# Performance work log

Measured on AMD Instinct MI355X. Metric: run time of the kernel, lower is better.

The kernel has to match this reference:

```python
import jax, jax.numpy as jnp
import numpy as np
import math

BLOCK = 256
NUM_HEADS = 32
HEAD_DIM = 128
HIDDEN = 2048
INNER = NUM_HEADS * HEAD_DIM
SEQ = 4096
EPS = 1e-5
LAYER_IDX = 0
NUM_LAYERS = 32


def _build_slopes(n):
    def get_slopes(n):
        def pow2(m):
            start = 2 ** (-2 ** (-(math.log2(m) - 3)))
            return [start * start ** i for i in range(m)]
        if math.log2(n).is_integer():
            return pow2(n)
        c = 2 ** math.floor(math.log2(n))
        return pow2(c) + get_slopes(2 * c)[0::2][: n - c]
    s = np.asarray(get_slopes(n), dtype=np.float32).reshape(n, 1, 1)
    # layer decay scaling as in __init__
    s = s * (1.0 - LAYER_IDX / (NUM_LAYERS - 1) + 1e-5)
    return s


def setup_inputs() -> dict:
    key = jax.random.key(0)
    k1, k2, k3, k4 = jax.random.split(key, 4)
    sd_h = 1.0 / math.sqrt(HIDDEN)
    sd_i = 1.0 / math.sqrt(INNER)
    return {
        "hidden_states": jax.random.normal(k1, (SEQ, HIDDEN), jnp.float32),
        "w_qkv": jax.random.normal(k2, (HIDDEN, 3 * INNER), jnp.float32) * sd_h,
        "w_gate": jax.random.normal(k3, (HIDDEN, INNER), jnp.float32) * sd_h,
        "w_out": jax.random.normal(k4, (INNER, HIDDEN), jnp.float32) * sd_i,
        "norm_weight": jnp.ones((INNER,), jnp.float32),
        "slope_rate": jnp.asarray(_build_slopes(NUM_HEADS)),
        "kv_cache": jnp.zeros((NUM_HEADS, HEAD_DIM, HEAD_DIM), jnp.float32),
    }


def _lightning_attention(q, k, v, slope, kv0):
    # q,k,v: [h, n, d]; slope: [h,1,1]; kv0: [h, d, d]
    h, n, d = q.shape
    nb = n // BLOCK
    qb = q.reshape(h, nb, BLOCK, d).transpose(1, 0, 2, 3)  # [nb,h,B,d]
    kb = k.reshape(h, nb, BLOCK, d).transpose(1, 0, 2, 3)
    vb = v.reshape(h, nb, BLOCK, d).transpose(1, 0, 2, 3)

    idx = jnp.arange(BLOCK, dtype=jnp.float32)
    diff = idx[:, None] - idx[None, :]                      # i - j
    s = slope.reshape(h, 1, 1)
    intra_decay = jnp.where(diff >= 0, jnp.exp(-s * diff), 0.0)   # [h,B,B]
    q_decay = jnp.exp(-s * (idx + 1.0).reshape(1, BLOCK, 1))      # [h,B,1]
    k_decay = jnp.exp(-s * (BLOCK - 1.0 - idx).reshape(1, BLOCK, 1))  # [h,B,1]
    block_decay = jnp.exp(-s * BLOCK)                             # [h,1,1]

    def step(kv, blk):
        qc, kc, vc = blk  # each [h,B,d]
        scores = jnp.einsum('hid,hjd->hij', qc, kc) * intra_decay
        o_intra = jnp.einsum('hij,hjd->hid', scores, vc)
        o_inter = q_decay * jnp.einsum('hid,hde->hie', qc, kv)
        kv_new = block_decay * kv + jnp.einsum('hjd,hje->hde', kc * k_decay, vc)
        return kv_new, o_intra + o_inter

    kv_final, outs = jax.lax.scan(step, kv0, (qb, kb, vb))
    out = outs.transpose(1, 0, 2, 3).reshape(h, n, d)
    return out, kv_final


def reference(hidden_states, w_qkv, w_gate, w_out, norm_weight, slope_rate, kv_cache):
    n = hidden_states.shape[0]
    # qkv projection + SiLU activation (done in fp32 in the original)
    qkv = jax.nn.silu(hidden_states @ w_qkv)                  # [n, 3*inner]
    qkv = qkv.reshape(n, NUM_HEADS, 3 * HEAD_DIM)
    q, k, v = jnp.split(qkv, 3, axis=-1)                      # [n,h,d] each
    q = q.transpose(1, 0, 2)                                  # [h,n,d]
    k = k.transpose(1, 0, 2)
    v = v.transpose(1, 0, 2)

    attn, kv_final = _lightning_attention(q, k, v, slope_rate, kv_cache)
    attn = attn.transpose(1, 0, 2).reshape(n, INNER)          # n (h d)

    # RMSNorm (fp32) then sigmoid gate then output projection
    var = jnp.mean(attn * attn, axis=-1, keepdims=True)
    normed = attn * jax.lax.rsqrt(var + EPS) * norm_weight
    gate = jax.nn.sigmoid(hidden_states @ w_gate)
    out = (gate * normed) @ w_out                             # [n, hidden]
    return out
```

## Files before the change

kernel.cpp:

```cpp
#include <hip/hip_runtime.h>
#include <stdint.h>

typedef __bf16 bf16x8 __attribute__((ext_vector_type(8)));
typedef float  f32x4  __attribute__((ext_vector_type(4)));
typedef unsigned short u16x8 __attribute__((ext_vector_type(8)));

__device__ __forceinline__ unsigned short f2bf(float f) {
    union { float f; uint32_t u; } x; x.f = f;
    uint32_t r = (x.u + 0x7FFFu + ((x.u >> 16) & 1u)) >> 16;
    return (unsigned short)r;
}
__device__ __forceinline__ float bf2f(unsigned short b) {
    union { uint32_t u; float f; } x; x.u = ((uint32_t)b) << 16;
    return x.f;
}

__device__ __forceinline__ void gl16(const void* g, void* l) {
    __builtin_amdgcn_global_load_lds(
        (const __attribute__((address_space(1))) void*)g,
        (__attribute__((address_space(3))) void*)(uint32_t)(uintptr_t)l,
        16, 0, 0);
}

#define MFMA16(a, b, c) __builtin_amdgcn_mfma_f32_16x16x32_bf16((a), (b), (c), 0, 0, 0)

__global__ __launch_bounds__(256) void f32_to_bf16_kernel(const float* __restrict__ in,
                                                          unsigned short* __restrict__ out,
                                                          int n8) {
    int i = blockIdx.x * 256 + threadIdx.x;
    if (i >= n8) return;
    float4 a = ((const float4*)in)[2 * i];
    float4 b = ((const float4*)in)[2 * i + 1];
    u16x8 o;
    o[0] = f2bf(a.x); o[1] = f2bf(a.y); o[2] = f2bf(a.z); o[3] = f2bf(a.w);
    o[4] = f2bf(b.x); o[5] = f2bf(b.y); o[6] = f2bf(b.z); o[7] = f2bf(b.w);
    ((u16x8*)out)[i] = o;
}

__global__ __launch_bounds__(256) void transpose_w_kernel(const float* __restrict__ in,
                                                          unsigned short* __restrict__ out,
                                                          int R, int C) {
    __shared__ float tile[32][33];
    int c0 = blockIdx.x * 32, r0 = blockIdx.y * 32;
    int lx = threadIdx.x & 31, ly = threadIdx.x >> 5;
#pragma unroll
    for (int i = ly; i < 32; i += 8)
        tile[i][lx] = in[(size_t)(r0 + i) * C + c0 + lx];
    __syncthreads();
#pragma unroll
    for (int i = ly; i < 32; i += 8)
        out[(size_t)(c0 + i) * R + r0 + lx] = f2bf(tile[lx][i]);
}

template <int ACT, int OUTF32>
__global__ __launch_bounds__(512, 2) void gemm256_kernel(const unsigned short* __restrict__ A,
                                                         const unsigned short* __restrict__ Bt,
                                                         void* __restrict__ Cout,
                                                         int N, int K, int NBN) {
    __shared__ unsigned short Abuf[2][2][8192];
    __shared__ unsigned short Bbuf[2][2][8192];

    int nwg = gridDim.x;
    int bid = blockIdx.x;
    int wg = (bid & 7) * (nwg >> 3) + (bid >> 3);
    int bm = wg / NBN, bn = wg % NBN;
    int tid = threadIdx.x, lane = tid & 63, w = tid >> 6;
    int wr = w >> 2, wc = w & 3;

    int r0 = tid >> 3;
    int cbs = (tid & 7) << 4;
    int el0 = (cbs ^ ((r0 & 7) << 4)) >> 1;
    int r1 = 64 + r0;
    int el1 = (cbs ^ ((r1 & 7) << 4)) >> 1;
    int lo0 = tid * 16, lo1 = 8192 + tid * 16;

    const unsigned short* Ag0 = A + (size_t)(bm * 256) * K;
    const unsigned short* Ag1 = A + (size_t)(bm * 256 + 128) * K;
    const unsigned short* Bg0 = Bt + (size_t)(bn * 256) * K;
    const unsigned short* Bg1 = Bt + (size_t)(bn * 256 + 128) * K;

#define STAGE(src, dstHalf, k0)                                            \
    do {                                                                   \
        gl16((src) + (size_t)r0 * K + (k0) + el0, (char*)(dstHalf) + lo0); \
        gl16((src) + (size_t)r1 * K + (k0) + el1, (char*)(dstHalf) + lo1); \
    } while (0)

    int aRow = wr * 64 + (lane & 15);
    int bRow = wc * 32 + (lane & 15);
    int swz = (lane & 7) << 4;
    int cbb = (lane >> 4) << 4;

#define RD_A(slot, R, m, kk) \
    af[R][m][kk] = *(const bf16x8*)((const char*)Abuf[slot][R] + ((aRow + (m) * 16) << 7) + (((kk) * 64 + cbb) ^ swz))
#define RD_B(slot, Cq, n, kk) \
    bfr[Cq][n][kk] = *(const bf16x8*)((const char*)Bbuf[slot][Cq] + ((bRow + (n) * 16) << 7) + (((kk) * 64 + cbb) ^ swz))

#define QUAD(q, Rh, Cc)                                                       \
    do {                                                                      \
        _Pragma("unroll")                                                     \
        for (int m = 0; m < 4; ++m)                                           \
            _Pragma("unroll")                                                 \
            for (int n = 0; n < 2; ++n) {                                     \
                acc[q][m][n] = MFMA16(af[Rh][m][0], bfr[Cc][n][0], acc[q][m][n]); \
                acc[q][m][n] = MFMA16(af[Rh][m][1], bfr[Cc][n][1], acc[q][m][n]); \
            }                                                                 \
    } while (0)

    bf16x8 af[2][4][2];
    bf16x8 bfr[2][2][2];
    f32x4 acc[4][4][2];
#pragma unroll
    for (int q = 0; q < 4; ++q)
#pragma unroll
        for (int m = 0; m < 4; ++m)
#pragma unroll
            for (int n = 0; n < 2; ++n)
#pragma unroll
                for (int r = 0; r < 4; ++r) acc[q][m][n][r] = 0.f;

    int NT = K >> 6;
    STAGE(Ag0, Abuf[0][0], 0);
    STAGE(Bg0, Bbuf[0][0], 0);
    STAGE(Ag1, Abuf[0][1], 0);
    STAGE(Bg1, Bbuf[0][1], 0);
    STAGE(Ag0, Abuf[1][0], 64);
    STAGE(Bg0, Bbuf[1][0], 64);
    STAGE(Ag1, Abuf[1][1], 64);
    STAGE(Bg1, Bbuf[1][1], 64);
    asm volatile("s_waitcnt vmcnt(8)" ::: "memory");
    __builtin_amdgcn_s_barrier();
#pragma unroll
    for (int m = 0; m < 4; ++m) { RD_A(0, 0, m, 0); RD_A(0, 0, m, 1); }
#pragma unroll
    for (int n = 0; n < 2; ++n) { RD_B(0, 0, n, 0); RD_B(0, 0, n, 1); }

    for (int t = 0; t < NT; ++t) {
        int cur = t & 1, nx = cur ^ 1;
        bool rd = (t + 1 < NT);
        bool st = (t + 2 < NT);
        int ks = (t + 2) << 6;

#pragma unroll
        for (int m = 0; m < 4; ++m) { RD_A(cur, 1, m, 0); RD_A(cur, 1, m, 1); }
        asm volatile("s_waitcnt lgkmcnt(8)" ::: "memory");
        __builtin_amdgcn_sched_barrier(0);
        __builtin_amdgcn_s_setprio(1);
        QUAD(0, 0, 0);
        __builtin_amdgcn_s_setprio(0);

#pragma unroll
        for (int n = 0; n < 2; ++n) { RD_B(cur, 1, n, 0); RD_B(cur, 1, n, 1); }
        asm volatile("s_waitcnt lgkmcnt(4)" ::: "memory");
        __builtin_amdgcn_sched_barrier(0);
        __builtin_amdgcn_s_setprio(1);
        QUAD(1, 1, 0);
        __builtin_amdgcn_s_setprio(0);

        asm volatile("s_waitcnt lgkmcnt(0)" ::: "memory");
        asm volatile("s_waitcnt vmcnt(0)" ::: "memory");
        __builtin_amdgcn_s_barrier();
        if (st) {
            STAGE(Ag0, Abuf[cur][0], ks);
            STAGE(Bg0, Bbuf[cur][0], ks);
        }
        if (rd) {
#pragma unroll
            for (int n = 0; n < 2; ++n) { RD_B(nx, 0, n, 0); RD_B(nx, 0, n, 1); }
        }
        __builtin_amdgcn_s_setprio(1);
        QUAD(2, 0, 1);
        __builtin_amdgcn_s_setprio(0);

        if (st) {
            STAGE(Ag1, Abuf[cur][1], ks);
            STAGE(Bg1, Bbuf[cur][1], ks);
        }
        if (rd) {
#pragma unroll
            for (int m = 0; m < 4; ++m) { RD_A(nx, 0, m, 0); RD_A(nx, 0, m, 1); }
        }
        __builtin_amdgcn_s_setprio(1);
        QUAD(3, 1, 1);
        __builtin_amdgcn_s_setprio(0);
    }

#pragma unroll
    for (int q = 0; q < 4; ++q) {
        const int R_ = q & 1, C_ = q >> 1;
#pragma unroll
        for (int m = 0; m < 4; ++m) {
            int row0 = bm * 256 + R_ * 128 + wr * 64 + m * 16 + ((lane >> 4) * 4);
#pragma unroll
            for (int n = 0; n < 2; ++n) {
                int col = bn * 256 + C_ * 128 + wc * 32 + n * 16 + (lane & 15);
#pragma unroll
                for (int rg = 0; rg < 4; ++rg) {
                    float v = acc[q][m][n][rg];
                    if (ACT == 1) v = v / (1.f + __expf(-v));
                    else if (ACT == 2) v = 1.f / (1.f + __expf(-v));
                    size_t idx = (size_t)(row0 + rg) * N + col;
                    if (OUTF32) ((float*)Cout)[idx] = v;
                    else        ((unsigned short*)Cout)[idx] = f2bf(v);
                }
            }
        }
    }
#undef STAGE
#undef RD_A
#undef RD_B
#undef QUAD
}

__global__ __launch_bounds__(256) void kv_transpose_kernel(const unsigned short* __restrict__ qkv,
                                                           const float* __restrict__ slopes,
                                                           unsigned short* __restrict__ kts,
                                                           unsigned short* __restrict__ vt) {
    __shared__ unsigned short tk[32][33];
    __shared__ unsigned short tv[32][33];
    int n0 = blockIdx.x * 32, d0 = blockIdx.y * 32, h = blockIdx.z;
    float s = slopes[h];
    int lx = threadIdx.x & 31, ly = threadIdx.x >> 5;
#pragma unroll
    for (int i = ly; i < 32; i += 8) {
        int n = n0 + i;
        size_t rowb = (size_t)n * 12288 + h * 384;
        float kv = bf2f(qkv[rowb + 128 + d0 + lx]) * __expf(-s * (float)(255 - (n & 255)));
        tk[i][lx] = f2bf(kv);
        tv[i][lx] = qkv[rowb + 256 + d0 + lx];
    }
    __syncthreads();
#pragma unroll
    for (int i = ly; i < 32; i += 8) {
        size_t ob = (size_t)(h * 128 + d0 + i) * 4096 + n0 + lx;
        kts[ob] = tk[lx][i];
        vt[ob] = tv[lx][i];
    }
}

__global__ __launch_bounds__(256) void kv_outer_kernel(const unsigned short* __restrict__ kts,
                                                       const unsigned short* __restrict__ vt,
                                                       float* __restrict__ U) {
    __shared__ unsigned short Kc[128 * 64];
    __shared__ unsigned short Vc[128 * 64];
    int blk = blockIdx.x;
    int h = blk & 31, t = blk >> 5;
    int tid = threadIdx.x, lane = tid & 63, w = tid >> 6;

    f32x4 acc[2][8];
#pragma unroll
    for (int m = 0; m < 2; ++m)
#pragma unroll
        for (int n = 0; n < 8; ++n)
#pragma unroll
            for (int r = 0; r < 4; ++r) acc[m][n][r] = 0.f;

    for (int ks = 0; ks < 4; ++ks) {
        __syncthreads();
#pragma unroll
        for (int it = 0; it < 4; ++it) {
            int slot = it * 256 + tid;
            int o = slot * 16;
            int r = o >> 7;
            int cb = o & 127;
            int scb = cb ^ ((r & 7) << 4);
            size_t j = (size_t)t * 256 + ks * 64 + (scb >> 1);
            gl16(kts + (size_t)(h * 128 + r) * 4096 + j, (char*)Kc + o);
            gl16(vt + (size_t)(h * 128 + r) * 4096 + j, (char*)Vc + o);
        }
        __syncthreads();
#pragma unroll
        for (int kk = 0; kk < 2; ++kk) {
            int kb = kk * 64 + ((lane >> 4) * 16);
            bf16x8 vf[2], kf[8];
#pragma unroll
            for (int m = 0; m < 2; ++m) {
                int e = w * 32 + m * 16 + (lane & 15);
                vf[m] = *(const bf16x8*)((const char*)Vc + (e << 7) + (kb ^ ((e & 7) << 4)));
            }
#pragma unroll
            for (int n = 0; n < 8; ++n) {
                int d = n * 16 + (lane & 15);
                kf[n] = *(const bf16x8*)((const char*)Kc + (d << 7) + (kb ^ ((d & 7) << 4)));
            }
#pragma unroll
            for (int m = 0; m < 2; ++m)
#pragma unroll
                for (int n = 0; n < 8; ++n)
                    acc[m][n] = MFMA16(vf[m], kf[n], acc[m][n]);
        }
    }
    size_t base = (size_t)(h * 16 + t) * 16384;
#pragma unroll
    for (int m = 0; m < 2; ++m)
#pragma unroll
        for (int n = 0; n < 8; ++n)
#pragma unroll
            for (int r = 0; r < 4; ++r) {
                int e = w * 32 + m * 16 + ((lane >> 4) * 4) + r;
                int d = n * 16 + (lane & 15);
                U[base + (size_t)e * 128 + d] = acc[m][n][r];
            }
}

__global__ __launch_bounds__(256) void kv_scan_kernel(const float* __restrict__ kv_cache,
                                                      const float* __restrict__ U,
                                                      const float* __restrict__ slopes,
                                                      unsigned short* __restrict__ Wb) {
    int h = blockIdx.x >> 3;
    int c0 = (blockIdx.x & 7) * 2048;
    int tid = threadIdx.x;
    float s = slopes[h];
    float bd = __expf(-s * 256.f);
    float wst[8];
    size_t hb = (size_t)h * 16384;
#pragma unroll
    for (int i = 0; i < 8; ++i) {
        int idx = c0 + i * 256 + tid;
        int e = idx >> 7, d = idx & 127;
        wst[i] = kv_cache[hb + (size_t)d * 128 + e];
    }
    for (int t = 0; t < 16; ++t) {
        size_t base = (size_t)(h * 16 + t) * 16384 + c0;
#pragma unroll
        for (int i = 0; i < 8; ++i) {
            int idx = i * 256 + tid;
            Wb[base + idx] = f2bf(wst[i]);
            wst[i] = bd * wst[i] + U[base + idx];
        }
    }
}

__global__ __launch_bounds__(256, 1) void attn_out_kernel(const unsigned short* __restrict__ qkv,
                                                          const unsigned short* __restrict__ vt,
                                                          const unsigned short* __restrict__ Wb,
                                                          const float* __restrict__ slopes,
                                                          unsigned short* __restrict__ attn) {
    __shared__ unsigned short lds[65536];
    unsigned short* Qs = lds;
    unsigned short* Ps = lds + 32768;
    unsigned short* KW = lds + 49152;
    unsigned short* Ks = KW;
    unsigned short* Vs = KW + 8192;

    int blk = blockIdx.x;
    int h = blk & 31, t = blk >> 5;
    float s = slopes[h];
    int tid = threadIdx.x, lane = tid & 63, w = tid >> 6;

#pragma unroll
    for (int it = 0; it < 16; ++it) {
        int slot = it * 256 + tid;
        int o = slot * 16;
        int r = o >> 8, cb = o & 255, scb = cb ^ ((r & 7) << 4);
        gl16(qkv + (size_t)(t * 256 + r) * 12288 + h * 384 + (scb >> 1), (char*)Qs + o);
    }
#pragma unroll
    for (int it = 0; it < 8; ++it) {
        int slot = it * 256 + tid;
        int o = slot * 16;
        int e = o >> 8, cb = o & 255, scb = cb ^ ((e & 7) << 4);
        gl16(Wb + (size_t)((h * 16 + t) * 128 + e) * 128 + (scb >> 1), (char*)KW + o);
    }
    __syncthreads();

    f32x4 acc[4][8];
#pragma unroll
    for (int m = 0; m < 4; ++m)
#pragma unroll
        for (int n = 0; n < 8; ++n)
#pragma unroll
            for (int r = 0; r < 4; ++r) acc[m][n][r] = 0.f;

#pragma unroll
    for (int kk = 0; kk < 4; ++kk) {
        int kb = kk * 64 + ((lane >> 4) * 16);
        bf16x8 qf[4], wf[8];
#pragma unroll
        for (int m = 0; m < 4; ++m) {
            int r = w * 64 + m * 16 + (lane & 15);
            qf[m] = *(const bf16x8*)((const char*)Qs + (r << 8) + (kb ^ ((r & 7) << 4)));
        }
#pragma unroll
        for (int n = 0; n < 8; ++n) {
            int e = n * 16 + (lane & 15);
            wf[n] = *(const bf16x8*)((const char*)KW + (e << 8) + (kb ^ ((e & 7) << 4)));
        }
#pragma unroll
        for (int m = 0; m < 4; ++m)
#pragma unroll
            for (int n = 0; n < 8; ++n)
                acc[m][n] = MFMA16(qf[m], wf[n], acc[m][n]);
    }
#pragma unroll
    for (int m = 0; m < 4; ++m)
#pragma unroll
        for (int rg = 0; rg < 4; ++rg) {
            int i = w * 64 + m * 16 + ((lane >> 4) * 4) + rg;
            float qd = __expf(-s * (float)(i + 1));
#pragma unroll
            for (int n = 0; n < 8; ++n) acc[m][n][rg] *= qd;
        }

    for (int jb = 0; jb < 4; ++jb) {
        __syncthreads();
#pragma unroll
        for (int it = 0; it < 4; ++it) {
            int slot = it * 256 + tid;
            int o = slot * 16;
            int r = o >> 8, cb = o & 255, scb = cb ^ ((r & 7) << 4);
            gl16(qkv + (size_t)(t * 256 + jb * 64 + r) * 12288 + h * 384 + 128 + (scb >> 1),
                 (char*)Ks + o);
        }
#pragma unroll
        for (int it = 0; it < 4; ++it) {
            int slot = it * 256 + tid;
            int o = slot * 16;
            int e = o >> 7, cb = o & 127, scb = cb ^ ((e & 7) << 4);
            gl16(vt + (size_t)(h * 128 + e) * 4096 + t * 256 + jb * 64 + (scb >> 1),
                 (char*)Vs + o);
        }
        __syncthreads();

        if (jb <= w) {
            f32x4 sc[4][4];
#pragma unroll
            for (int m = 0; m < 4; ++m)
#pragma unroll
                for (int n = 0; n < 4; ++n)
#pragma unroll
                    for (int r = 0; r < 4; ++r) sc[m][n][r] = 0.f;
#pragma unroll
            for (int kk = 0; kk < 4; ++kk) {
                int kb = kk * 64 + ((lane >> 4) * 16);
                bf16x8 qf[4], kf[4];
#pragma unroll
                for (int m = 0; m < 4; ++m) {
                    int r = w * 64 + m * 16 + (lane & 15);
                    qf[m] = *(const bf16x8*)((const char*)Qs + (r << 8) + (kb ^ ((r & 7) << 4)));
                }
#pragma unroll
                for (int n = 0; n < 4; ++n) {
                    int r = n * 16 + (lane & 15);
                    kf[n] = *(const bf16x8*)((const char*)Ks + (r << 8) + (kb ^ ((r & 7) << 4)));
                }
#pragma unroll
                for (int m = 0; m < 4; ++m)
#pragma unroll
                    for (int n = 0; n < 4; ++n)
                        sc[m][n] = MFMA16(qf[m], kf[n], sc[m][n]);
            }
            unsigned short* Pw = Ps + w * 4096;
#pragma unroll
            for (int m = 0; m < 4; ++m)
#pragma unroll
                for (int n = 0; n < 4; ++n)
#pragma unroll
                    for (int rg = 0; rg < 4; ++rg) {
                        int il = m * 16 + ((lane >> 4) * 4) + rg;
                        int i = w * 64 + il;
                        int jl = n * 16 + (lane & 15);
                        int j = jb * 64 + jl;
                        float v = 0.f;
                        if (i >= j) v = sc[m][n][rg] * __expf(-s * (float)(i - j));
                        int cb2 = (jl * 2) ^ ((il & 7) << 4);
                        *(unsigned short*)((char*)Pw + (il << 7) + cb2) = f2bf(v);
                    }
            asm volatile("s_waitcnt lgkmcnt(0)" ::: "memory");
#pragma unroll
            for (int kk = 0; kk < 2; ++kk) {
                int kb = kk * 64 + ((lane >> 4) * 16);
                bf16x8 pf[4], vf[8];
#pragma unroll
                for (int m = 0; m < 4; ++m) {
                    int il = m * 16 + (lane & 15);
                    pf[m] = *(const bf16x8*)((const char*)Pw + (il << 7) + (kb ^ ((il & 7) << 4)));
                }
#pragma unroll
                for (int n = 0; n < 8; ++n) {
                    int e = n * 16 + (lane & 15);
                    vf[n] = *(const bf16x8*)((const char*)Vs + (e << 7) + (kb ^ ((e & 7) << 4)));
                }
#pragma unroll
                for (int m = 0; m < 4; ++m)
#pragma unroll
                    for (int n = 0; n < 8; ++n)
                        acc[m][n] = MFMA16(pf[m], vf[n], acc[m][n]);
            }
        }
    }

#pragma unroll
    for (int m = 0; m < 4; ++m)
#pragma unroll
        for (int n = 0; n < 8; ++n)
#pragma unroll
            for (int rg = 0; rg < 4; ++rg) {
                int i = w * 64 + m * 16 + ((lane >> 4) * 4) + rg;
                int col = h * 128 + n * 16 + (lane & 15);
                attn[(size_t)(t * 256 + i) * 4096 + col] = f2bf(acc[m][n][rg]);
            }
}

__global__ __launch_bounds__(256) void rms_gate_kernel(const unsigned short* __restrict__ attn,
                                                       const unsigned short* __restrict__ gate,
                                                       const float* __restrict__ nw,
                                                       unsigned short* __restrict__ gated) {
    int row = blockIdx.x, tid = threadIdx.x;
    int lane = tid & 63, w = tid >> 6;
    const unsigned short* ar = attn + (size_t)row * 4096 + tid * 16;
    u16x8 a0 = *(const u16x8*)ar;
    u16x8 a1 = *(const u16x8*)(ar + 8);
    float v[16];
    float ss = 0.f;
#pragma unroll
    for (int j = 0; j < 8; ++j) { v[j] = bf2f(a0[j]); v[8 + j] = bf2f(a1[j]); }
#pragma unroll
    for (int j = 0; j < 16; ++j) ss += v[j] * v[j];
#pragma unroll
    for (int o = 32; o > 0; o >>= 1) ss += __shfl_xor(ss, o);
    __shared__ float red[4];
    if (lane == 0) red[w] = ss;
    __syncthreads();
    float tot = red[0] + red[1] + red[2] + red[3];
    float rs = rsqrtf(tot * (1.f / 4096.f) + 1e-5f);
    const unsigned short* gr = gate + (size_t)row * 4096 + tid * 16;
    u16x8 g0 = *(const u16x8*)gr;
    u16x8 g1 = *(const u16x8*)(gr + 8);
    const float* nwp = nw + tid * 16;
    u16x8 o0, o1;
#pragma unroll
    for (int j = 0; j < 8; ++j) {
        o0[j] = f2bf(v[j] * rs * nwp[j] * bf2f(g0[j]));
        o1[j] = f2bf(v[8 + j] * rs * nwp[8 + j] * bf2f(g1[j]));
    }
    unsigned short* gp = gated + (size_t)row * 4096 + tid * 16;
    *(u16x8*)gp = o0;
    *(u16x8*)(gp + 8) = o1;
}

extern "C" void kernel_launch(void* const* d_in, const int* in_sizes, int n_in,
                              void* d_out, int out_size, void* d_ws, size_t ws_size,
                              hipStream_t stream) {
    const float* hs       = (const float*)d_in[0];
    const float* w_qkv    = (const float*)d_in[1];
    const float* w_gate   = (const float*)d_in[2];
    const float* w_out    = (const float*)d_in[3];
    const float* nw       = (const float*)d_in[4];
    const float* slopes   = (const float*)d_in[5];
    const float* kv_cache = (const float*)d_in[6];
    float* out = (float*)d_out;
    char* ws = (char*)d_ws;

    unsigned short* hsb  = (unsigned short*)(ws + 0);
    unsigned short* wqt  = (unsigned short*)(ws + 16777216);
    unsigned short* wgt  = (unsigned short*)(ws + 67108864);
    unsigned short* wot  = (unsigned short*)(ws + 83886080);
    unsigned short* qkv  = (unsigned short*)(ws + 100663296);
    unsigned short* gate = (unsigned short*)(ws + 201326592);
    unsigned short* kts  = (unsigned short*)(ws + 234881024);
    unsigned short* vt   = (unsigned short*)(ws + 268435456);
    float*          U    = (float*)(ws + 301989888);
    unsigned short* Wb   = (unsigned short*)(ws + 335544320);
    unsigned short* attn  = wqt;
    unsigned short* gated = qkv;

    f32_to_bf16_kernel<<<4096, 256, 0, stream>>>(hs, hsb, 1048576);
    {
        dim3 g(384, 64);
        transpose_w_kernel<<<g, 256, 0, stream>>>(w_qkv, wqt, 2048, 12288);
    }
    {
        dim3 g(128, 64);
        transpose_w_kernel<<<g, 256, 0, stream>>>(w_gate, wgt, 2048, 4096);
    }
    {
        dim3 g(64, 128);
        transpose_w_kernel<<<g, 256, 0, stream>>>(w_out, wot, 4096, 2048);
    }
    gemm256_kernel<1, 0><<<768, 512, 0, stream>>>(hsb, wqt, qkv, 12288, 2048, 48);
    gemm256_kernel<2, 0><<<256, 512, 0, stream>>>(hsb, wgt, gate, 4096, 2048, 16);
    {
        dim3 g(128, 4, 32);
        kv_transpose_kernel<<<g, 256, 0, stream>>>(qkv, slopes, kts, vt);
    }
    kv_outer_kernel<<<512, 256, 0, stream>>>(kts, vt, U);
    kv_scan_kernel<<<256, 256, 0, stream>>>(kv_cache, U, slopes, Wb);
    attn_out_kernel<<<512, 256, 0, stream>>>(qkv, vt, Wb, slopes, attn);
    rms_gate_kernel<<<4096, 256, 0, stream>>>(attn, gate, nw, gated);
    gemm256_kernel<0, 1><<<128, 512, 0, stream>>>(gated, wot, out, 2048, 4096, 8);
}
```

Before: 567.1 us.

## Remap GEMM tiles, split attention query tiles, add small-tile output GEMM

The large GEMM's block-to-tile mapping is changed so that each XCD covers a compact group of M and N tiles, which should improve L2 reuse. The output projection moves from a 128-block 256x256 GEMM to a new 128x128-tile GEMM with 512 blocks, so more CUs are busy; the new kernel has no double buffering. attn_out now splits each 256-row query block into two 128-row halves, doubling the grid and halving LDS so two blocks fit per CU. kv_scan stages the transposed kv_cache read through LDS so the global loads are coalesced.

```diff
diff --git a/kernel.cpp b/kernel.cpp
--- a/kernel.cpp
+++ b/kernel.cpp
@@ -60,10 +60,10 @@
     __shared__ unsigned short Abuf[2][2][8192];
     __shared__ unsigned short Bbuf[2][2][8192];
 
-    int nwg = gridDim.x;
     int bid = blockIdx.x;
-    int wg = (bid & 7) * (nwg >> 3) + (bid >> 3);
-    int bm = wg / NBN, bn = wg % NBN;
+    int xcd = bid & 7, kw = bid >> 3;
+    int bm = (xcd & 3) * 4 + (kw & 3);
+    int bn = (xcd >> 2) * (NBN >> 1) + (kw >> 2);
     int tid = threadIdx.x, lane = tid & 63, w = tid >> 6;
     int wr = w >> 2, wc = w & 3;
 
@@ -211,6 +211,82 @@
 #undef QUAD
 }
 
+template <int ACT, int OUTBF>
+__global__ __launch_bounds__(256) void gemm_bt_kernel(const unsigned short* __restrict__ A,
+                                                      const unsigned short* __restrict__ Bt,
+                                                      void* __restrict__ Cp,
+                                                      int M, int N, int K) {
+    __shared__ unsigned short As[128 * 64];
+    __shared__ unsigned short Bs[128 * 64];
+    int bn = blockIdx.x, bm = blockIdx.y;
+    int tid = threadIdx.x, lane = tid & 63, w = tid >> 6;
+    int wr = w >> 1, wc = w & 1;
+
+    f32x4 acc[4][4];
+#pragma unroll
+    for (int m = 0; m < 4; ++m)
+#pragma unroll
+        for (int n = 0; n < 4; ++n)
+#pragma unroll
+            for (int r = 0; r < 4; ++r) acc[m][n][r] = 0.f;
+
+    const size_t Abase = (size_t)bm * 128 * K;
+    const size_t Bbase = (size_t)bn * 128 * K;
+
+    for (int k0 = 0; k0 < K; k0 += 64) {
+        __syncthreads();
+#pragma unroll
+        for (int it = 0; it < 4; ++it) {
+            int slot = it * 256 + tid;
+            int o = slot * 16;
+            int r = o >> 7;
+            int cb = o & 127;
+            int scb = cb ^ ((r & 7) << 4);
+            gl16(A + Abase + (size_t)r * K + k0 + (scb >> 1), (char*)As + o);
+            gl16(Bt + Bbase + (size_t)r * K + k0 + (scb >> 1), (char*)Bs + o);
+        }
+        __syncthreads();
+#pragma unroll
+        for (int kk = 0; kk < 2; ++kk) {
+            int kb = kk * 64 + ((lane >> 4) * 16);
+            bf16x8 af[4], bfr[4];
+#pragma unroll
+            for (int m = 0; m < 4; ++m) {
+                int r = wr * 64 + m * 16 + (lane & 15);
+                af[m] = *(const bf16x8*)((const char*)As + (r << 7) + (kb ^ ((r & 7) << 4)));
+            }
+#pragma unroll
+            for (int n = 0; n < 4; ++n) {
+                int r = wc * 64 + n * 16 + (lane & 15);
+                bfr[n] = *(const bf16x8*)((const char*)Bs + (r << 7) + (kb ^ ((r & 7) << 4)));
+            }
+#pragma unroll
+            for (int m = 0; m < 4; ++m)
+#pragma unroll
+                for (int n = 0; n < 4; ++n)
+                    acc[m][n] = MFMA16(af[m], bfr[n], acc[m][n]);
+        }
+    }
+
+#pragma unroll
+    for (int m = 0; m < 4; ++m) {
+        int rowb = bm * 128 + wr * 64 + m * 16 + ((lane >> 4) * 4);
+#pragma unroll
+        for (int n = 0; n < 4; ++n) {
+            int col = bn * 128 + wc * 64 + n * 16 + (lane & 15);
+#pragma unroll
+            for (int r = 0; r < 4; ++r) {
+                float v = acc[m][n][r];
+                if (ACT == 1) v = v / (1.f + __expf(-v));
+                else if (ACT == 2) v = 1.f / (1.f + __expf(-v));
+                size_t idx = (size_t)(rowb + r) * N + col;
+                if (OUTBF) ((unsigned short*)Cp)[idx] = f2bf(v);
+                else       ((float*)Cp)[idx] = v;
+            }
+        }
+    }
+}
+
 __global__ __launch_bounds__(256) void kv_transpose_kernel(const unsigned short* __restrict__ qkv,
                                                            const float* __restrict__ slopes,
                                                            unsigned short* __restrict__ kts,
@@ -306,18 +382,25 @@
                                                       const float* __restrict__ U,
                                                       const float* __restrict__ slopes,
                                                       unsigned short* __restrict__ Wb) {
+    __shared__ float Tt[16][132];
     int h = blockIdx.x >> 3;
-    int c0 = (blockIdx.x & 7) * 2048;
+    int c = blockIdx.x & 7;
+    int c0 = c * 2048, e0 = c * 16;
     int tid = threadIdx.x;
     float s = slopes[h];
     float bd = __expf(-s * 256.f);
+    size_t hb = (size_t)h * 16384;
+#pragma unroll
+    for (int it = 0; it < 8; ++it) {
+        int d = it * 16 + (tid >> 4);
+        Tt[tid & 15][d] = kv_cache[hb + (size_t)d * 128 + e0 + (tid & 15)];
+    }
+    __syncthreads();
     float wst[8];
-    size_t hb = (size_t)h * 16384;
 #pragma unroll
     for (int i = 0; i < 8; ++i) {
-        int idx = c0 + i * 256 + tid;
-        int e = idx >> 7, d = idx & 127;
-        wst[i] = kv_cache[hb + (size_t)d * 128 + e];
+        int e_rel = i * 2 + (tid >> 7);
+        wst[i] = Tt[e_rel][tid & 127];
     }
     for (int t = 0; t < 16; ++t) {
         size_t base = (size_t)(h * 16 + t) * 16384 + c0;
@@ -330,42 +413,42 @@
     }
 }
 
-__global__ __launch_bounds__(256, 1) void attn_out_kernel(const unsigned short* __restrict__ qkv,
+__global__ __launch_bounds__(256, 2) void attn_out_kernel(const unsigned short* __restrict__ qkv,
                                                           const unsigned short* __restrict__ vt,
                                                           const unsigned short* __restrict__ Wb,
                                                           const float* __restrict__ slopes,
                                                           unsigned short* __restrict__ attn) {
-    __shared__ unsigned short lds[65536];
+    __shared__ unsigned short lds[40960];
     unsigned short* Qs = lds;
-    unsigned short* Ps = lds + 32768;
-    unsigned short* KW = lds + 49152;
+    unsigned short* Ps = lds + 16384;
+    unsigned short* KW = lds + 24576;
     unsigned short* Ks = KW;
     unsigned short* Vs = KW + 8192;
 
     int blk = blockIdx.x;
-    int h = blk & 31, t = blk >> 5;
+    int h = blk & 31, tq = blk >> 5;
+    int t = tq >> 1, qh = tq & 1;
     float s = slopes[h];
     int tid = threadIdx.x, lane = tid & 63, w = tid >> 6;
-
-#pragma unroll
-    for (int it = 0; it < 16; ++it) {
-        int slot = it * 256 + tid;
-        int o = slot * 16;
+    int rowbase = t * 256 + qh * 128;
+
+#pragma unroll
+    for (int it = 0; it < 8; ++it) {
+        int o = (it * 256 + tid) * 16;
         int r = o >> 8, cb = o & 255, scb = cb ^ ((r & 7) << 4);
-        gl16(qkv + (size_t)(t * 256 + r) * 12288 + h * 384 + (scb >> 1), (char*)Qs + o);
+        gl16(qkv + (size_t)(rowbase + r) * 12288 + h * 384 + (scb >> 1), (char*)Qs + o);
     }
 #pragma unroll
     for (int it = 0; it < 8; ++it) {
-        int slot = it * 256 + tid;
-        int o = slot * 16;
+        int o = (it * 256 + tid) * 16;
         int e = o >> 8, cb = o & 255, scb = cb ^ ((e & 7) << 4);
         gl16(Wb + (size_t)((h * 16 + t) * 128 + e) * 128 + (scb >> 1), (char*)KW + o);
     }
     __syncthreads();
 
-    f32x4 acc[4][8];
-#pragma unroll
-    for (int m = 0; m < 4; ++m)
+    f32x4 acc[2][8];
+#pragma unroll
+    for (int m = 0; m < 2; ++m)
 #pragma unroll
         for (int n = 0; n < 8; ++n)
 #pragma unroll
@@ -374,10 +457,10 @@
 #pragma unroll
     for (int kk = 0; kk < 4; ++kk) {
         int kb = kk * 64 + ((lane >> 4) * 16);
-        bf16x8 qf[4], wf[8];
-#pragma unroll
-        for (int m = 0; m < 4; ++m) {
-            int r = w * 64 + m * 16 + (lane & 15);
+        bf16x8 qf[2], wf[8];
+#pragma unroll
+        for (int m = 0; m < 2; ++m) {
+            int r = w * 32 + m * 16 + (lane & 15);
             qf[m] = *(const bf16x8*)((const char*)Qs + (r << 8) + (kb ^ ((r & 7) << 4)));
         }
 #pragma unroll
@@ -386,45 +469,44 @@
             wf[n] = *(const bf16x8*)((const char*)KW + (e << 8) + (kb ^ ((e & 7) << 4)));
         }
 #pragma unroll
-        for (int m = 0; m < 4; ++m)
+        for (int m = 0; m < 2; ++m)
 #pragma unroll
             for (int n = 0; n < 8; ++n)
                 acc[m][n] = MFMA16(qf[m], wf[n], acc[m][n]);
     }
 #pragma unroll
-    for (int m = 0; m < 4; ++m)
+    for (int m = 0; m < 2; ++m)
 #pragma unroll
         for (int rg = 0; rg < 4; ++rg) {
-            int i = w * 64 + m * 16 + ((lane >> 4) * 4) + rg;
+            int i = qh * 128 + w * 32 + m * 16 + ((lane >> 4) * 4) + rg;
             float qd = __expf(-s * (float)(i + 1));
 #pragma unroll
             for (int n = 0; n < 8; ++n) acc[m][n][rg] *= qd;
         }
 
+    int jbmax = ((qh << 2) + w) >> 1;
     for (int jb = 0; jb < 4; ++jb) {
         __syncthreads();
 #pragma unroll
         for (int it = 0; it < 4; ++it) {
-            int slot = it * 256 + tid;
-            int o = slot * 16;
+            int o = (it * 256 + tid) * 16;
             int r = o >> 8, cb = o & 255, scb = cb ^ ((r & 7) << 4);
             gl16(qkv + (size_t)(t * 256 + jb * 64 + r) * 12288 + h * 384 + 128 + (scb >> 1),
                  (char*)Ks + o);
         }
 #pragma unroll
         for (int it = 0; it < 4; ++it) {
-            int slot = it * 256 + tid;
-            int o = slot * 16;
+            int o = (it * 256 + tid) * 16;
             int e = o >> 7, cb = o & 127, scb = cb ^ ((e & 7) << 4);
             gl16(vt + (size_t)(h * 128 + e) * 4096 + t * 256 + jb * 64 + (scb >> 1),
                  (char*)Vs + o);
         }
         __syncthreads();
 
-        if (jb <= w) {
-            f32x4 sc[4][4];
-#pragma unroll
-            for (int m = 0; m < 4; ++m)
+        if (jb <= jbmax) {
+            f32x4 sc[2][4];
+#pragma unroll
+            for (int m = 0; m < 2; ++m)
 #pragma unroll
                 for (int n = 0; n < 4; ++n)
 #pragma unroll
@@ -432,10 +514,10 @@
 #pragma unroll
             for (int kk = 0; kk < 4; ++kk) {
                 int kb = kk * 64 + ((lane >> 4) * 16);
-                bf16x8 qf[4], kf[4];
-#pragma unroll
-                for (int m = 0; m < 4; ++m) {
-                    int r = w * 64 + m * 16 + (lane & 15);
+                bf16x8 qf[2], kf[4];
+#pragma unroll
+                for (int m = 0; m < 2; ++m) {
+                    int r = w * 32 + m * 16 + (lane & 15);
                     qf[m] = *(const bf16x8*)((const char*)Qs + (r << 8) + (kb ^ ((r & 7) << 4)));
                 }
 #pragma unroll
@@ -444,20 +526,20 @@
                     kf[n] = *(const bf16x8*)((const char*)Ks + (r << 8) + (kb ^ ((r & 7) << 4)));
                 }
 #pragma unroll
-                for (int m = 0; m < 4; ++m)
+                for (int m = 0; m < 2; ++m)
 #pragma unroll
                     for (int n = 0; n < 4; ++n)
                         sc[m][n] = MFMA16(qf[m], kf[n], sc[m][n]);
             }
-            unsigned short* Pw = Ps + w * 4096;
-#pragma unroll
-            for (int m = 0; m < 4; ++m)
+            unsigned short* Pw = Ps + w * 2048;
+#pragma unroll
+            for (int m = 0; m < 2; ++m)
 #pragma unroll
                 for (int n = 0; n < 4; ++n)
 #pragma unroll
                     for (int rg = 0; rg < 4; ++rg) {
                         int il = m * 16 + ((lane >> 4) * 4) + rg;
-                        int i = w * 64 + il;
+                        int i = qh * 128 + w * 32 + il;
                         int jl = n * 16 + (lane & 15);
                         int j = jb * 64 + jl;
                         float v = 0.f;
@@ -469,9 +551,9 @@
 #pragma unroll
             for (int kk = 0; kk < 2; ++kk) {
                 int kb = kk * 64 + ((lane >> 4) * 16);
-                bf16x8 pf[4], vf[8];
-#pragma unroll
-                for (int m = 0; m < 4; ++m) {
+                bf16x8 pf[2], vf[8];
+#pragma unroll
+                for (int m = 0; m < 2; ++m) {
                     int il = m * 16 + (lane & 15);
                     pf[m] = *(const bf16x8*)((const char*)Pw + (il << 7) + (kb ^ ((il & 7) << 4)));
                 }
@@ -481,7 +563,7 @@
                     vf[n] = *(const bf16x8*)((const char*)Vs + (e << 7) + (kb ^ ((e & 7) << 4)));
                 }
 #pragma unroll
-                for (int m = 0; m < 4; ++m)
+                for (int m = 0; m < 2; ++m)
 #pragma unroll
                     for (int n = 0; n < 8; ++n)
                         acc[m][n] = MFMA16(pf[m], vf[n], acc[m][n]);
@@ -490,12 +572,12 @@
     }
 
 #pragma unroll
-    for (int m = 0; m < 4; ++m)
+    for (int m = 0; m < 2; ++m)
 #pragma unroll
         for (int n = 0; n < 8; ++n)
 #pragma unroll
             for (int rg = 0; rg < 4; ++rg) {
-                int i = w * 64 + m * 16 + ((lane >> 4) * 4) + rg;
+                int i = qh * 128 + w * 32 + m * 16 + ((lane >> 4) * 4) + rg;
                 int col = h * 128 + n * 16 + (lane & 15);
                 attn[(size_t)(t * 256 + i) * 4096 + col] = f2bf(acc[m][n][rg]);
             }
@@ -585,7 +667,10 @@
     }
     kv_outer_kernel<<<512, 256, 0, stream>>>(kts, vt, U);
     kv_scan_kernel<<<256, 256, 0, stream>>>(kv_cache, U, slopes, Wb);
-    attn_out_kernel<<<512, 256, 0, stream>>>(qkv, vt, Wb, slopes, attn);
+    attn_out_kernel<<<1024, 256, 0, stream>>>(qkv, vt, Wb, slopes, attn);
     rms_gate_kernel<<<4096, 256, 0, stream>>>(attn, gate, nw, gated);
-    gemm256_kernel<0, 1><<<128, 512, 0, stream>>>(gated, wot, out, 2048, 4096, 8);
-}
+    {
+        dim3 g(16, 32);
+        gemm_bt_kernel<0, 0><<<g, 256, 0, stream>>>(gated, wot, out, 4096, 2048, 4096);
+    }
+}
```

Result: faster. 539.2 us (-4.9%).
